# Kernel optimization log

Hardware: AMD Instinct MI355X
Metric: run time of the kernel (lower is better)

## Reference

```python
import jax, jax.numpy as jnp
import numpy as np

B, C, D, H, W = 2, 64, 8, 24, 24  # hidden_dim = C; N = D*H*W = 4608 tokens


def setup_inputs() -> dict:
    key = jax.random.key(0)
    ks = jax.random.split(key, 8)
    s = 1.0 / np.sqrt(C)  # fan-in style init for 1x1 conv weights
    return {
        "x": jax.random.normal(ks[0], (B, C, D, H, W), dtype=jnp.float32),
        "h": jax.random.normal(ks[1], (B, C, D, H, W), dtype=jnp.float32),
        "Wq": jax.random.normal(ks[2], (C, C), dtype=jnp.float32) * s,
        "bq": jax.random.normal(ks[3], (C,), dtype=jnp.float32) * s,
        "Wk": jax.random.normal(ks[4], (C, C), dtype=jnp.float32) * s,
        "bk": jax.random.normal(ks[5], (C,), dtype=jnp.float32) * s,
        "Wv": jax.random.normal(ks[6], (C, C), dtype=jnp.float32) * s,
        "bv": jax.random.normal(ks[7], (C,), dtype=jnp.float32) * s,
    }


def reference(x, h, Wq, bq, Wk, bk, Wv, bv):
    # 1x1 Conv3d == per-token linear over channels
    def proj(inp, Wt, bt):
        f = inp.reshape(inp.shape[0], inp.shape[1], -1)  # [B, C, N]
        return jnp.einsum('oc,bcn->bon', Wt, f) + bt[None, :, None]

    q = proj(x, Wq, bq)  # [B, C, N]
    k = proj(h, Wk, bk)  # [B, C, N]
    v = proj(h, Wv, bv)  # [B, C, N]

    scale = 1.0 / np.sqrt(k.shape[1])  # k.size(1) ** 0.5 == sqrt(C)
    scores = jnp.einsum('bcm,bcn->bmn', q, k) * scale  # [B, N, N]
    attn = jax.nn.softmax(scores, axis=-1)
    out = jnp.einsum('bcn,bmn->bcm', v, attn)  # [B, C, N]
    return out.reshape(h.shape)
```

## Files before the change

kernel.cpp:

```cpp
#include <hip/hip_runtime.h>
#include <hip/hip_bf16.h>

#define C_DIM 64
#define N_TOK 4608
#define NBLK  72
#define B_SZ  2
#define M64BLKS 72
#define NSEG  8
#define SEGLEN (N_TOK / NSEG)
#define NT32  (SEGLEN / 32)
#define KTILES 288
#define VTILES 72
#define OSTR  68

typedef __bf16 bf16x8 __attribute__((ext_vector_type(8)));
typedef float  f32x4  __attribute__((ext_vector_type(4)));


__device__ __forceinline__ void gll16(const void* g, void* l) {
    __builtin_amdgcn_global_load_lds(
        (const __attribute__((address_space(1))) void*)g,
        (__attribute__((address_space(3))) void*)l, 16, 0, 0);
}

__device__ __forceinline__ void gemm_tile(
    const __hip_bfloat16* wmat, const bf16x8 bin[2], const float* bias,
    int col, int quad, f32x4 acc[4])
{
    #pragma unroll
    for (int ot = 0; ot < 4; ot++) {
        f32x4 a = (f32x4){0.f, 0.f, 0.f, 0.f};
        #pragma unroll
        for (int kh = 0; kh < 2; kh++) {
            bf16x8 wf = *(const bf16x8*)(wmat + (ot * 16 + col) * 72 +
                                         kh * 32 + quad * 8);
            a = __builtin_amdgcn_mfma_f32_16x16x32_bf16(wf, bin[kh], a, 0, 0, 0);
        }
        float4 b4 = *(const float4*)(bias + ot * 16 + quad * 4);
        a[0] += b4.x; a[1] += b4.y; a[2] += b4.z; a[3] += b4.w;
        acc[ot] = a;
    }
}

__global__ __launch_bounds__(256) void proj_kernel(
    const float* __restrict__ x,  const float* __restrict__ h,
    const float* __restrict__ Wq, const float* __restrict__ bq,
    const float* __restrict__ Wk, const float* __restrict__ bk,
    const float* __restrict__ Wv, const float* __restrict__ bv,
    __hip_bfloat16* __restrict__ qS, __hip_bfloat16* __restrict__ kS,
    __hip_bfloat16* __restrict__ vS)
{
    __shared__ __hip_bfloat16 wl[3 * 64 * 72];
    __shared__ __hip_bfloat16 xt[64 * 72];
    __shared__ __hip_bfloat16 ht[64 * 72];
    __shared__ __hip_bfloat16 vl[64 * 72];

    const int b  = blockIdx.x / NBLK;
    const int n0 = (blockIdx.x % NBLK) * 64;
    const int t  = threadIdx.x;

    #pragma unroll
    for (int mat = 0; mat < 3; mat++) {
        const float* W = (mat == 0) ? Wq : ((mat == 1) ? Wk : Wv);
        __hip_bfloat16* wd = wl + mat * (64 * 72);
        #pragma unroll
        for (int i = 0; i < 4; i++) {
            const int ch = i * 256 + t;
            const int o = ch >> 4, c0 = (ch & 15) * 4;
            float4 w4 = *(const float4*)(W + ch * 4);
            union { __hip_bfloat16 e[4]; uint2 v; } pk;
            pk.e[0] = __float2bfloat16(w4.x); pk.e[1] = __float2bfloat16(w4.y);
            pk.e[2] = __float2bfloat16(w4.z); pk.e[3] = __float2bfloat16(w4.w);
            *(uint2*)(wd + o * 72 + c0) = pk.v;
        }
    }
    #pragma unroll
    for (int i = 0; i < 4; i++) {
        const int ch = i * 256 + t;
        const int c = ch >> 4, n4 = (ch & 15) * 4;
        float4 x4 = *(const float4*)(x + (size_t)(b * C_DIM + c) * N_TOK + n0 + n4);
        float4 h4 = *(const float4*)(h + (size_t)(b * C_DIM + c) * N_TOK + n0 + n4);
        xt[(n4 + 0) * 72 + c] = __float2bfloat16(x4.x);
        xt[(n4 + 1) * 72 + c] = __float2bfloat16(x4.y);
        xt[(n4 + 2) * 72 + c] = __float2bfloat16(x4.z);
        xt[(n4 + 3) * 72 + c] = __float2bfloat16(x4.w);
        ht[(n4 + 0) * 72 + c] = __float2bfloat16(h4.x);
        ht[(n4 + 1) * 72 + c] = __float2bfloat16(h4.y);
        ht[(n4 + 2) * 72 + c] = __float2bfloat16(h4.z);
        ht[(n4 + 3) * 72 + c] = __float2bfloat16(h4.w);
    }
    __syncthreads();

    const int wave = t >> 6, lane = t & 63;
    const int col = lane & 15, quad = lane >> 4;

    bf16x8 xb[2], hb[2];
    #pragma unroll
    for (int kh = 0; kh < 2; kh++) {
        xb[kh] = *(const bf16x8*)(xt + (wave * 16 + col) * 72 + kh * 32 + quad * 8);
        hb[kh] = *(const bf16x8*)(ht + (wave * 16 + col) * 72 + kh * 32 + quad * 8);
    }

    f32x4 acc[4];

    gemm_tile(wl + 0 * (64 * 72), xb, bq, col, quad, acc);
    {
        const size_t tile16 = (size_t)b * KTILES + (n0 >> 4) + wave;
        const float SC = 0.125f * 1.44269504088896f;
        #pragma unroll
        for (int ot = 0; ot < 4; ot++) {
            union { __hip_bfloat16 e[4]; uint2 v; } pk;
            #pragma unroll
            for (int r = 0; r < 4; r++) pk.e[r] = __float2bfloat16(acc[ot][r] * SC);
            *(uint2*)(qS + (tile16 << 10) + (ot >> 1) * 512 +
                      ((ot * 2 + (quad >> 1)) & 3) * 128 + col * 8 +
                      (quad & 1) * 4) = pk.v;
        }
    }

    gemm_tile(wl + 1 * (64 * 72), hb, bk, col, quad, acc);
    {
        const int t_l = (wave >> 1) * 2 + ((col >> 2) & 1);
        const int row = ((wave * 2 + (col >> 3)) & 3) * 4 + (col & 3);
        const size_t tile16 = (size_t)b * KTILES + (n0 >> 4) + t_l;
        #pragma unroll
        for (int ot = 0; ot < 4; ot++) {
            union { __hip_bfloat16 e[4]; uint2 v; } pk;
            #pragma unroll
            for (int r = 0; r < 4; r++) pk.e[r] = __float2bfloat16(acc[ot][r]);
            *(uint2*)(kS + (tile16 << 10) + (ot >> 1) * 512 +
                      ((ot * 2 + (quad >> 1)) & 3) * 128 + row * 8 +
                      (quad & 1) * 4) = pk.v;
        }
    }

    gemm_tile(wl + 2 * (64 * 72), hb, bv, col, quad, acc);
    #pragma unroll
    for (int ot = 0; ot < 4; ot++)
        #pragma unroll
        for (int r = 0; r < 4; r++)
            vl[(ot * 16 + quad * 4 + r) * 72 + wave * 16 + col] =
                __float2bfloat16(acc[ot][r]);
    __syncthreads();
    {
        const size_t vbase = ((size_t)(b * VTILES) + (n0 >> 6)) << 12;
        #pragma unroll
        for (int rep = 0; rep < 2; rep++) {
            const int ch = rep * 256 + t;
            const int cc = ch >> 7, hf = (ch >> 6) & 1;
            const int qd = (ch >> 4) & 3, c2 = ch & 15;
            *(uint4*)(vS + vbase + (size_t)ch * 8) =
                *(const uint4*)(vl + (cc * 16 + c2) * 72 + hf * 32 + qd * 8);
        }
    }
}

__global__ __launch_bounds__(512) void attn_kernel(
    const __hip_bfloat16* __restrict__ qS,
    const __hip_bfloat16* __restrict__ kS,
    const __hip_bfloat16* __restrict__ vS,
    float* __restrict__ out)
{
    __shared__ __align__(16) char smem[NSEG * 16384];
    float* o_lds = (float*)smem;
    float* lstat = (float*)(smem + NSEG * 16 * OSTR * 4);

    const int b    = blockIdx.x / M64BLKS;
    const int mblk = blockIdx.x % M64BLKS;
    const int wave = threadIdx.x >> 6;
    const int lane = threadIdx.x & 63;
    const int col  = lane & 15;
    const int quad = lane >> 4;
    const int m0   = mblk * 64;

    const __hip_bfloat16* qp =
        qS + (((size_t)b * KTILES + (m0 >> 4)) << 10) + lane * 8;
    bf16x8 qa[4][2];
    #pragma unroll
    for (int ms = 0; ms < 4; ms++) {
        qa[ms][0] = *(const bf16x8*)(qp + ms * 1024);
        qa[ms][1] = *(const bf16x8*)(qp + ms * 1024 + 512);
    }

    f32x4 accO[4][4];
    #pragma unroll
    for (int ms = 0; ms < 4; ms++)
        #pragma unroll
        for (int cc = 0; cc < 4; cc++)
            accO[ms][cc] = (f32x4){0.f, 0.f, 0.f, 0.f};
    float rsum[4] = {0.f, 0.f, 0.f, 0.f};

    const int nbeg = wave * SEGLEN;
    char* sbase = smem + wave * 16384;
    const __hip_bfloat16* kbb = kS + (((size_t)b * KTILES) << 10) + lane * 8;
    const __hip_bfloat16* vbb = vS + (((size_t)b * VTILES) << 12) + lane * 8;

    auto stage = [&](int t, int p) {
        const int n0 = nbeg + t * 32;
        char* dst = sbase + p * 8192;
        const __hip_bfloat16* kt = kbb + ((size_t)(n0 >> 4) << 10);
        #pragma unroll
        for (int j = 0; j < 2; j++) {
            gll16(kt + (j << 10),       dst + j * 2048);
            gll16(kt + (j << 10) + 512, dst + j * 2048 + 1024);
        }
        const __hip_bfloat16* vt = vbb + ((size_t)(n0 >> 6) << 12) +
                                   ((n0 >> 5) & 1) * 512;
        #pragma unroll
        for (int cc = 0; cc < 4; cc++)
            gll16(vt + cc * 1024, dst + 4096 + cc * 1024);
    };

    stage(0, 0);

    #pragma unroll 1
    for (int t = 0; t < NT32; t++) {
        const int p = t & 1;
        if (t + 1 < NT32) {
            stage(t + 1, p ^ 1);
            asm volatile("s_waitcnt vmcnt(8)" ::: "memory");
        } else {
            asm volatile("s_waitcnt vmcnt(0)" ::: "memory");
        }
        __builtin_amdgcn_sched_barrier(0);

        const char* buf = sbase + p * 8192;
        bf16x8 ka[4], va[4];
        #pragma unroll
        for (int j = 0; j < 2; j++) {
            ka[2 * j]     = *(const bf16x8*)(buf + j * 2048 + lane * 16);
            ka[2 * j + 1] = *(const bf16x8*)(buf + j * 2048 + 1024 + lane * 16);
        }
        #pragma unroll
        for (int cc = 0; cc < 4; cc++)
            va[cc] = *(const bf16x8*)(buf + 4096 + cc * 1024 + lane * 16);

        #pragma unroll
        for (int ms = 0; ms < 4; ms++) {
            f32x4 s0 = __builtin_amdgcn_mfma_f32_16x16x32_bf16(
                           ka[0], qa[ms][0], (f32x4){0.f, 0.f, 0.f, 0.f}, 0, 0, 0);
            s0 = __builtin_amdgcn_mfma_f32_16x16x32_bf16(ka[1], qa[ms][1], s0, 0, 0, 0);
            f32x4 s1 = __builtin_amdgcn_mfma_f32_16x16x32_bf16(
                           ka[2], qa[ms][0], (f32x4){0.f, 0.f, 0.f, 0.f}, 0, 0, 0);
            s1 = __builtin_amdgcn_mfma_f32_16x16x32_bf16(ka[3], qa[ms][1], s1, 0, 0, 0);

            union { __hip_bfloat16 e[8]; bf16x8 v; } pk;
            float ps = 0.f;
            #pragma unroll
            for (int r = 0; r < 4; r++) {
                float e0 = __builtin_amdgcn_exp2f(s0[r]);
                float e1 = __builtin_amdgcn_exp2f(s1[r]);
                ps += e0 + e1;
                pk.e[r]     = __float2bfloat16(e0);
                pk.e[4 + r] = __float2bfloat16(e1);
            }
            rsum[ms] += ps;
            #pragma unroll
            for (int cc = 0; cc < 4; cc++)
                accO[ms][cc] = __builtin_amdgcn_mfma_f32_16x16x32_bf16(
                                   va[cc], pk.v, accO[ms][cc], 0, 0, 0);
        }
    }

    #pragma unroll
    for (int ms = 0; ms < 4; ms++) {
        rsum[ms] += __shfl_xor(rsum[ms], 16);
        rsum[ms] += __shfl_xor(rsum[ms], 32);
    }

    __syncthreads();

    if (quad == 0) {
        #pragma unroll
        for (int ms = 0; ms < 4; ms++) lstat[wave * 64 + ms * 16 + col] = rsum[ms];
    }

    #pragma unroll
    for (int phase = 0; phase < 4; phase++) {
        #pragma unroll
        for (int cc = 0; cc < 4; cc++)
            *(f32x4*)(o_lds + (wave * 16 + col) * OSTR + cc * 16 + quad * 4) =
                accO[phase][cc];
        __syncthreads();
        if (threadIdx.x < 256) {
            const int m  = threadIdx.x & 15;
            const int cq = threadIdx.x >> 4;
            const int mi = phase * 16 + m;
            float lsum = 0.f;
            f32x4 oacc = (f32x4){0.f, 0.f, 0.f, 0.f};
            #pragma unroll
            for (int sgm = 0; sgm < NSEG; sgm++) {
                lsum += lstat[sgm * 64 + mi];
                oacc += *(const f32x4*)(o_lds + (sgm * 16 + m) * OSTR + cq * 4);
            }
            const float inv = 1.0f / lsum;
            #pragma unroll
            for (int r = 0; r < 4; r++) {
                const int c = cq * 4 + r;
                out[(size_t)(b * C_DIM + c) * N_TOK + m0 + phase * 16 + m] =
                    oacc[r] * inv;
            }
        }
        __syncthreads();
    }
}

extern "C" void kernel_launch(void* const* d_in, const int* in_sizes, int n_in,
                              void* d_out, int out_size, void* d_ws, size_t ws_size,
                              hipStream_t stream) {
    const float* x  = (const float*)d_in[0];
    const float* h  = (const float*)d_in[1];
    const float* Wq = (const float*)d_in[2];
    const float* bq = (const float*)d_in[3];
    const float* Wk = (const float*)d_in[4];
    const float* bk = (const float*)d_in[5];
    const float* Wv = (const float*)d_in[6];
    const float* bv = (const float*)d_in[7];
    float* out = (float*)d_out;

    const size_t elems = (size_t)B_SZ * N_TOK * C_DIM;
    __hip_bfloat16* qS = (__hip_bfloat16*)d_ws;
    __hip_bfloat16* kS = qS + elems;
    __hip_bfloat16* vS = kS + elems;

    proj_kernel<<<B_SZ * NBLK, 256, 0, stream>>>(x, h, Wq, bq, Wk, bk, Wv, bv,
                                                 qS, kS, vS);
    attn_kernel<<<B_SZ * M64BLKS, 512, 0, stream>>>(qS, kS, vS, out);
}
```

Baseline: 95.78 us.

## Split attention block across 16 waves and load K/V directly to registers

```diff
diff --git a/kernel.cpp b/kernel.cpp
--- a/kernel.cpp
+++ b/kernel.cpp
@@ -16,12 +16,6 @@
 typedef __bf16 bf16x8 __attribute__((ext_vector_type(8)));
 typedef float  f32x4  __attribute__((ext_vector_type(4)));
 
-
-__device__ __forceinline__ void gll16(const void* g, void* l) {
-    __builtin_amdgcn_global_load_lds(
-        (const __attribute__((address_space(1))) void*)g,
-        (__attribute__((address_space(3))) void*)l, 16, 0, 0);
-}
 
 __device__ __forceinline__ void gemm_tile(
     const __hip_bfloat16* wmat, const bf16x8 bin[2], const float* bias,
@@ -155,15 +149,14 @@
     }
 }
 
-__global__ __launch_bounds__(512) void attn_kernel(
+__global__ __launch_bounds__(1024) void attn_kernel(
     const __hip_bfloat16* __restrict__ qS,
     const __hip_bfloat16* __restrict__ kS,
     const __hip_bfloat16* __restrict__ vS,
     float* __restrict__ out)
 {
-    __shared__ __align__(16) char smem[NSEG * 16384];
-    float* o_lds = (float*)smem;
-    float* lstat = (float*)(smem + NSEG * 16 * OSTR * 4);
+    __shared__ float o_lds[2][NSEG][16][OSTR];
+    __shared__ float lstat[2][NSEG][32];
 
     const int b    = blockIdx.x / M64BLKS;
     const int mblk = blockIdx.x % M64BLKS;
@@ -172,71 +165,49 @@
     const int col  = lane & 15;
     const int quad = lane >> 4;
     const int m0   = mblk * 64;
+    const int mg   = wave >> 3;
+    const int seg  = wave & 7;
 
     const __hip_bfloat16* qp =
-        qS + (((size_t)b * KTILES + (m0 >> 4)) << 10) + lane * 8;
-    bf16x8 qa[4][2];
-    #pragma unroll
-    for (int ms = 0; ms < 4; ms++) {
+        qS + (((size_t)b * KTILES + (m0 >> 4) + mg * 2) << 10) + lane * 8;
+    bf16x8 qa[2][2];
+    #pragma unroll
+    for (int ms = 0; ms < 2; ms++) {
         qa[ms][0] = *(const bf16x8*)(qp + ms * 1024);
         qa[ms][1] = *(const bf16x8*)(qp + ms * 1024 + 512);
     }
 
-    f32x4 accO[4][4];
-    #pragma unroll
-    for (int ms = 0; ms < 4; ms++)
+    f32x4 accO[2][4];
+    #pragma unroll
+    for (int ms = 0; ms < 2; ms++)
         #pragma unroll
         for (int cc = 0; cc < 4; cc++)
             accO[ms][cc] = (f32x4){0.f, 0.f, 0.f, 0.f};
-    float rsum[4] = {0.f, 0.f, 0.f, 0.f};
-
-    const int nbeg = wave * SEGLEN;
-    char* sbase = smem + wave * 16384;
+    float rsum[2] = {0.f, 0.f};
+
+    const int nbeg = seg * SEGLEN;
     const __hip_bfloat16* kbb = kS + (((size_t)b * KTILES) << 10) + lane * 8;
     const __hip_bfloat16* vbb = vS + (((size_t)b * VTILES) << 12) + lane * 8;
 
-    auto stage = [&](int t, int p) {
+    #pragma unroll 1
+    for (int t = 0; t < NT32; t++) {
         const int n0 = nbeg + t * 32;
-        char* dst = sbase + p * 8192;
         const __hip_bfloat16* kt = kbb + ((size_t)(n0 >> 4) << 10);
+        bf16x8 ka[4];
         #pragma unroll
         for (int j = 0; j < 2; j++) {
-            gll16(kt + (j << 10),       dst + j * 2048);
-            gll16(kt + (j << 10) + 512, dst + j * 2048 + 1024);
+            ka[2 * j]     = *(const bf16x8*)(kt + (j << 10));
+            ka[2 * j + 1] = *(const bf16x8*)(kt + (j << 10) + 512);
         }
         const __hip_bfloat16* vt = vbb + ((size_t)(n0 >> 6) << 12) +
                                    ((n0 >> 5) & 1) * 512;
+        bf16x8 va[4];
         #pragma unroll
         for (int cc = 0; cc < 4; cc++)
-            gll16(vt + cc * 1024, dst + 4096 + cc * 1024);
-    };
-
-    stage(0, 0);
-
-    #pragma unroll 1
-    for (int t = 0; t < NT32; t++) {
-        const int p = t & 1;
-        if (t + 1 < NT32) {
-            stage(t + 1, p ^ 1);
-            asm volatile("s_waitcnt vmcnt(8)" ::: "memory");
-        } else {
-            asm volatile("s_waitcnt vmcnt(0)" ::: "memory");
-        }
-        __builtin_amdgcn_sched_barrier(0);
-
-        const char* buf = sbase + p * 8192;
-        bf16x8 ka[4], va[4];
-        #pragma unroll
-        for (int j = 0; j < 2; j++) {
-            ka[2 * j]     = *(const bf16x8*)(buf + j * 2048 + lane * 16);
-            ka[2 * j + 1] = *(const bf16x8*)(buf + j * 2048 + 1024 + lane * 16);
-        }
-        #pragma unroll
-        for (int cc = 0; cc < 4; cc++)
-            va[cc] = *(const bf16x8*)(buf + 4096 + cc * 1024 + lane * 16);
-
-        #pragma unroll
-        for (int ms = 0; ms < 4; ms++) {
+            va[cc] = *(const bf16x8*)(vt + cc * 1024);
+
+        #pragma unroll
+        for (int ms = 0; ms < 2; ms++) {
             f32x4 s0 = __builtin_amdgcn_mfma_f32_16x16x32_bf16(
                            ka[0], qa[ms][0], (f32x4){0.f, 0.f, 0.f, 0.f}, 0, 0, 0);
             s0 = __builtin_amdgcn_mfma_f32_16x16x32_bf16(ka[1], qa[ms][1], s0, 0, 0, 0);
@@ -263,42 +234,40 @@
     }
 
     #pragma unroll
-    for (int ms = 0; ms < 4; ms++) {
+    for (int ms = 0; ms < 2; ms++) {
         rsum[ms] += __shfl_xor(rsum[ms], 16);
         rsum[ms] += __shfl_xor(rsum[ms], 32);
     }
-
-    __syncthreads();
-
     if (quad == 0) {
         #pragma unroll
-        for (int ms = 0; ms < 4; ms++) lstat[wave * 64 + ms * 16 + col] = rsum[ms];
-    }
-
-    #pragma unroll
-    for (int phase = 0; phase < 4; phase++) {
+        for (int ms = 0; ms < 2; ms++) lstat[mg][seg][ms * 16 + col] = rsum[ms];
+    }
+
+    #pragma unroll
+    for (int phase = 0; phase < 2; phase++) {
         #pragma unroll
         for (int cc = 0; cc < 4; cc++)
-            *(f32x4*)(o_lds + (wave * 16 + col) * OSTR + cc * 16 + quad * 4) =
+            *(f32x4*)(&o_lds[mg][seg][col][cc * 16 + quad * 4]) =
                 accO[phase][cc];
         __syncthreads();
-        if (threadIdx.x < 256) {
-            const int m  = threadIdx.x & 15;
-            const int cq = threadIdx.x >> 4;
-            const int mi = phase * 16 + m;
+        if (threadIdx.x < 512) {
+            const int g  = threadIdx.x >> 8;
+            const int r8 = threadIdx.x & 255;
+            const int m  = r8 & 15;
+            const int cq = r8 >> 4;
             float lsum = 0.f;
             f32x4 oacc = (f32x4){0.f, 0.f, 0.f, 0.f};
             #pragma unroll
             for (int sgm = 0; sgm < NSEG; sgm++) {
-                lsum += lstat[sgm * 64 + mi];
-                oacc += *(const f32x4*)(o_lds + (sgm * 16 + m) * OSTR + cq * 4);
+                lsum += lstat[g][sgm][phase * 16 + m];
+                oacc += *(const f32x4*)(&o_lds[g][sgm][m][cq * 4]);
             }
             const float inv = 1.0f / lsum;
+            const int mglob = m0 + g * 32 + phase * 16 + m;
             #pragma unroll
             for (int r = 0; r < 4; r++) {
                 const int c = cq * 4 + r;
-                out[(size_t)(b * C_DIM + c) * N_TOK + m0 + phase * 16 + m] =
-                    oacc[r] * inv;
+                out[(size_t)(b * C_DIM + c) * N_TOK + mglob] = oacc[r] * inv;
             }
         }
         __syncthreads();
@@ -325,5 +294,5 @@
 
     proj_kernel<<<B_SZ * NBLK, 256, 0, stream>>>(x, h, Wq, bq, Wk, bk, Wv, bv,
                                                  qS, kS, vS);
-    attn_kernel<<<B_SZ * M64BLKS, 512, 0, stream>>>(qS, kS, vS, out);
-}
+    attn_kernel<<<B_SZ * M64BLKS, 1024, 0, stream>>>(qS, kS, vS, out);
+}
```

Result: no change. 96.98 us (+1.3%).
